# Kernel tuning notes

Measured on AMD Instinct MI355X. Metric: run time of the kernel, lower is better.

Reference implementation:

```python
import jax, jax.numpy as jnp
import numpy as np

B, C, H, W = 8, 192, 128, 128
NH, WS, PS = 6, 8, 8
HD = C // NH
SCALE = HD ** -0.5

def _rel_pos_log(ws):
    # log-spaced signed relative coordinates, [N, N, 2]
    coords = np.stack(np.meshgrid(np.arange(ws), np.arange(ws), indexing='ij'))
    cf = coords.reshape(2, -1)
    rp = (cf[:, :, None] - cf[:, None, :]).transpose(1, 2, 0).astype(np.float32)
    return jnp.asarray(np.sign(rp) * np.log1p(np.abs(rp)))

def setup_inputs() -> dict:
    key = jax.random.key(0)
    ks = jax.random.split(key, 8)
    s = 0.02
    return {
        'x': jax.random.normal(ks[0], (B, C, H, W), jnp.float32),
        'V_w': jax.random.normal(ks[1], (C, C), jnp.float32) * s,
        'V_b': jnp.zeros((C,), jnp.float32),
        'QK_w': jax.random.normal(ks[2], (2 * C, C), jnp.float32) * s,
        'QK_b': jnp.zeros((2 * C,), jnp.float32),
        'proj_w': jax.random.normal(ks[3], (C, C), jnp.float32) * s,
        'proj_b': jnp.zeros((C,), jnp.float32),
        'meta_w1': jax.random.normal(ks[4], (2, 256), jnp.float32) * s,
        'meta_b1': jnp.zeros((256,), jnp.float32),
        'meta_w2': jax.random.normal(ks[5], (256, NH), jnp.float32) * s,
        'meta_b2': jnp.zeros((NH,), jnp.float32),
    }

def reference(x, V_w, V_b, QK_w, QK_b, proj_w, proj_b, meta_w1, meta_b1, meta_w2, meta_b2):
    N = WS * WS
    # 1x1 convs for V and QK
    v = jnp.einsum('bchw,oc->bohw', x, V_w) + V_b[None, :, None, None]
    qk = jnp.einsum('bchw,oc->bohw', x, QK_w) + QK_b[None, :, None, None]
    qkv = jnp.concatenate([qk, v], axis=1)  # [B, 3C, H, W]
    # window partition -> [B * nW, N, 3C]
    t = qkv.transpose(0, 2, 3, 1).reshape(B, H // WS, WS, W // WS, WS, 3 * C)
    wins = t.transpose(0, 1, 3, 2, 4, 5).reshape(-1, N, 3 * C)
    B_ = wins.shape[0]
    qkv3 = wins.reshape(B_, N, 3, NH, HD).transpose(2, 0, 3, 1, 4)
    q, k, vv = qkv3[0] * SCALE, qkv3[1], qkv3[2]  # [B_, NH, N, HD]
    # FFT cross-modulation of q and k over the 8x8 window grid (c = N/64 = 1)
    cg = N // (PS * PS)
    qp = q.reshape(B_, NH, cg, PS, PS, HD).transpose(0, 1, 2, 5, 3, 4)
    kp = k.reshape(B_, NH, cg, PS, PS, HD).transpose(0, 1, 2, 5, 3, 4)
    o = jnp.fft.irfft2(jnp.fft.rfft2(qp) * jnp.fft.rfft2(kp), s=(PS, PS))
    o = o.transpose(0, 1, 2, 4, 5, 3).reshape(B_, NH, N, HD)
    # relative position bias from meta MLP on log-spaced coords
    rp = _rel_pos_log(WS)  # [N, N, 2]
    bias = jax.nn.relu(rp @ meta_w1 + meta_b1) @ meta_w2 + meta_b2  # [N, N, NH]
    bias = bias.transpose(2, 0, 1)  # [NH, N, N]
    attn = jnp.einsum('bhnd,bhmd->bhnm', o, vv) + bias[None]
    attn = jax.nn.softmax(attn, axis=-1)
    y = jnp.einsum('bhnm,bhmd->bhnd', attn, vv).transpose(0, 2, 1, 3).reshape(B_, N, C)
    # window reverse -> [B, C, H, W]
    y = y.reshape(B, H // WS, W // WS, WS, WS, C).transpose(0, 1, 3, 2, 4, 5).reshape(B, H, W, C)
    y = y.transpose(0, 3, 1, 2)
    return jnp.einsum('bchw,oc->bohw', y, proj_w) + proj_b[None, :, None, None]
```

## Files before the change

kernel.cpp:

```cpp
#include <hip/hip_runtime.h>

#define SCALEQ 0.17677669529663687f

typedef __bf16 bf16x8 __attribute__((ext_vector_type(8)));
typedef __bf16 bf16x2 __attribute__((ext_vector_type(2)));
typedef float f32x4 __attribute__((ext_vector_type(4)));
typedef float f32x2 __attribute__((ext_vector_type(2)));

__device__ __forceinline__ float bflo(unsigned int u) { return __uint_as_float(u << 16); }
__device__ __forceinline__ float bfhi(unsigned int u) { return __uint_as_float(u & 0xffff0000u); }
__device__ __forceinline__ f32x2 b2x2(unsigned int u) {
    f32x2 r; r[0] = bflo(u); r[1] = bfhi(u); return r;
}
__device__ __forceinline__ unsigned short f2b(float f) {
    return __builtin_bit_cast(unsigned short, (__bf16)f);
}
__device__ __forceinline__ unsigned int pk2(float a, float b) {
    bf16x2 v; v[0] = (__bf16)a; v[1] = (__bf16)b;
    return __builtin_bit_cast(unsigned int, v);
}

#define RA     0
#define RB     24576
#define RC     49152
#define LDS_BYTES 73728

#define WS_WQKV_ELEMS 110592
#define WS_WP_OFF_EL  110592
#define WS_B2_OFF_B   294912

__device__ __forceinline__ bf16x8 ldsf(const char* p) {
    uint4 u = *(const uint4*)p;
    return __builtin_bit_cast(bf16x8, u);
}
__device__ __forceinline__ bf16x8 gldf(const unsigned short* p) {
    uint4 u = *(const uint4*)p;
    return __builtin_bit_cast(bf16x8, u);
}

__global__ void wprep_kernel(const float* __restrict__ QKw, const float* __restrict__ Vw,
                             const float* __restrict__ Pw, unsigned short* __restrict__ wsb) {
    int i = blockIdx.x * 256 + threadIdx.x;
    if (i >= 147456) return;
    if (i < WS_WQKV_ELEMS) {
        int r = i / 192, c = i - r * 192;
        float v = (r < 384) ? QKw[r * 192 + c] : Vw[(r - 384) * 192 + c];
        if (r < 192) v *= SCALEQ;
        wsb[i] = f2b(v);
    } else {
        int j = i - WS_WQKV_ELEMS;
        wsb[WS_WP_OFF_EL + j] = f2b(Pw[j]);
    }
}

__global__ void bias2_kernel(const float* __restrict__ Mw1, const float* __restrict__ Mb1,
                             const float* __restrict__ Mw2, const float* __restrict__ Mb2,
                             float* __restrict__ out) {
    int i = blockIdx.x * 256 + threadIdx.x;
    if (i >= 6 * 64 * 64) return;
    int h = i >> 12, n = (i >> 6) & 63, m = i & 63;
    float dy = (float)((n >> 3) - (m >> 3));
    float dx = (float)((n & 7) - (m & 7));
    float f0 = copysignf(log1pf(fabsf(dy)), dy);
    float f1 = copysignf(log1pf(fabsf(dx)), dx);
    float a = Mb2[h];
    for (int u = 0; u < 256; ++u) {
        float hv = fmaxf(f0 * Mw1[u] + f1 * Mw1[256 + u] + Mb1[u], 0.0f);
        a = fmaf(hv, Mw2[u * 6 + h], a);
    }
    out[i] = a;
}

__global__ __launch_bounds__(512, 4)
void fused_win_attn(const float* __restrict__ x,
                    const float* __restrict__ Vb, const float* __restrict__ QKb,
                    const float* __restrict__ Pb,
                    const unsigned short* __restrict__ wqkv,
                    const unsigned short* __restrict__ wp,
                    const float* __restrict__ bias2,
                    float* __restrict__ out)
{
    extern __shared__ char smem[];
    const int t   = threadIdx.x;
    const int wv  = t >> 6;
    const int l15 = t & 15;
    const int l4  = (t >> 4) & 3;

    const int wid = ((blockIdx.x & 7) << 8) | (blockIdx.x >> 3);
    const int b   = wid >> 8;
    const int wy  = (wid >> 4) & 15;
    const int wx  = wid & 15;
    const int y0  = wy * 8, x0 = wx * 8;

    const f32x4 zz = {0.0f, 0.0f, 0.0f, 0.0f};

    {
        const float* xb = x + (size_t)b * 192 * 16384;
        #pragma unroll
        for (int i = 0; i < 6; ++i) {
            int idx = t + 512 * i;
            int c = idx >> 4, sub = idx & 15;
            int r = sub >> 1, hf = sub & 1;
            float4 v4 = *(const float4*)(xb + c * 16384 + (y0 + r) * 128 + x0 + hf * 4);
            int n0 = r * 8 + hf * 4;
            unsigned short sv[4] = {f2b(v4.x), f2b(v4.y), f2b(v4.z), f2b(v4.w)};
            #pragma unroll
            for (int e = 0; e < 4; ++e) {
                int n = n0 + e;
                *(unsigned short*)(smem + RA + ((n * 384 + c * 2) ^ ((n & 7) << 4))) = sv[e];
            }
        }
    }
    __syncthreads();

    const int wcol = wv & 3, wrow = wv >> 2;
    unsigned int vp[3][2][2];
    {
        bf16x8 afr[6][2];
        #pragma unroll
        for (int ks = 0; ks < 6; ++ks)
            #pragma unroll
            for (int mtl = 0; mtl < 2; ++mtl) {
                int row = (wrow * 2 + mtl) * 16 + l15;
                afr[ks][mtl] = ldsf(smem + RA + ((row * 384 + ks * 64 + l4 * 16) ^ ((row & 7) << 4)));
            }
        __syncthreads();

        auto gemm3 = [&](int obase, f32x4 acc[3][2]) {
            bf16x8 bw[3][6];
            #pragma unroll
            for (int j = 0; j < 3; ++j) {
                const unsigned short* wr = wqkv + (size_t)(obase + j * 16 + l15) * 192 + l4 * 8;
                #pragma unroll
                for (int ks = 0; ks < 6; ++ks) bw[j][ks] = gldf(wr + ks * 32);
            }
            #pragma unroll
            for (int j = 0; j < 3; ++j) { acc[j][0] = zz; acc[j][1] = zz; }
            #pragma unroll
            for (int ks = 0; ks < 6; ++ks)
                #pragma unroll
                for (int j = 0; j < 3; ++j)
                    #pragma unroll
                    for (int mtl = 0; mtl < 2; ++mtl)
                        acc[j][mtl] = __builtin_amdgcn_mfma_f32_16x16x32_bf16(afr[ks][mtl], bw[j][ks], acc[j][mtl], 0, 0, 0);
        };

        {
            f32x4 acc[3][2];
            gemm3(wcol * 48, acc);
            #pragma unroll
            for (int j = 0; j < 3; ++j) {
                int och = wcol * 48 + j * 16 + l15;
                float bv = QKb[och] * SCALEQ;
                #pragma unroll
                for (int mtl = 0; mtl < 2; ++mtl)
                    #pragma unroll
                    for (int rr = 0; rr < 4; ++rr) {
                        int tok = (wrow * 2 + mtl) * 16 + l4 * 4 + rr;
                        *(unsigned short*)(smem + RA + ((tok * 384 + och * 2) ^ ((tok & 7) << 4)))
                            = f2b(acc[j][mtl][rr] + bv);
                    }
            }
        }
        {
            f32x4 acc[3][2];
            gemm3(192 + wcol * 48, acc);
            #pragma unroll
            for (int j = 0; j < 3; ++j) {
                int ch = wcol * 48 + j * 16 + l15;
                float bv = QKb[192 + ch];
                #pragma unroll
                for (int mtl = 0; mtl < 2; ++mtl)
                    #pragma unroll
                    for (int rr = 0; rr < 4; ++rr) {
                        int tok = (wrow * 2 + mtl) * 16 + l4 * 4 + rr;
                        *(unsigned short*)(smem + RB + ((tok * 384 + ch * 2) ^ ((tok & 7) << 4)))
                            = f2b(acc[j][mtl][rr] + bv);
                    }
            }
        }
        {
            f32x4 acc[3][2];
            gemm3(384 + wcol * 48, acc);
            #pragma unroll
            for (int j = 0; j < 3; ++j) {
                int ch = wcol * 48 + j * 16 + l15;
                float bv = Vb[ch];
                #pragma unroll
                for (int mtl = 0; mtl < 2; ++mtl) {
                    vp[j][mtl][0] = pk2(acc[j][mtl][0] + bv, acc[j][mtl][1] + bv);
                    vp[j][mtl][1] = pk2(acc[j][mtl][2] + bv, acc[j][mtl][3] + bv);
                }
            }
        }
    }
    __syncthreads();

    if (t < 384) {
        const int rn = t / 48, cc = t % 48;
        const int c0b = cc * 8;
        f32x2 acc[8][2];
        #pragma unroll
        for (int cn = 0; cn < 8; ++cn) {
            acc[cn][0] = (f32x2){0.0f, 0.0f};
            acc[cn][1] = (f32x2){0.0f, 0.0f};
        }
        #pragma unroll
        for (int kh = 0; kh < 2; ++kh) {
            uint2 karr[32];
            #pragma unroll
            for (int m = 0; m < 32; ++m) {
                int row = kh * 32 + m;
                karr[m] = *(const uint2*)(smem + RB + ((row * 384 + c0b) ^ ((row & 7) << 4)));
            }
            #pragma unroll
            for (int mrl = 0; mrl < 4; ++mrl) {
                const int mr = kh * 4 + mrl;
                f32x2 kf[8][2];
                #pragma unroll
                for (int mc = 0; mc < 8; ++mc) {
                    uint2 kv = karr[mrl * 8 + mc];
                    kf[mc][0] = b2x2(kv.x); kf[mc][1] = b2x2(kv.y);
                }
                const int npr = (rn - mr) & 7;
                #pragma unroll
                for (int npc = 0; npc < 8; ++npc) {
                    int np = npr * 8 + npc;
                    uint2 qv = *(const uint2*)(smem + RA + ((np * 384 + c0b) ^ ((np & 7) << 4)));
                    f32x2 qf0 = b2x2(qv.x), qf1 = b2x2(qv.y);
                    #pragma unroll
                    for (int mc = 0; mc < 8; ++mc) {
                        int cn = (npc + mc) & 7;
                        acc[cn][0] = qf0 * kf[mc][0] + acc[cn][0];
                        acc[cn][1] = qf1 * kf[mc][1] + acc[cn][1];
                    }
                }
            }
        }
        #pragma unroll
        for (int cn = 0; cn < 8; ++cn) {
            int n = rn * 8 + cn;
            uint2 pk;
            pk.x = pk2(acc[cn][0][0], acc[cn][0][1]);
            pk.y = pk2(acc[cn][1][0], acc[cn][1][1]);
            *(uint2*)(smem + RC + ((n * 384 + c0b) ^ ((n & 7) << 4))) = pk;
        }
    }
    __syncthreads();

    {
        #pragma unroll
        for (int j = 0; j < 3; ++j) {
            int ch = wcol * 48 + j * 16 + l15;
            #pragma unroll
            for (int mtl = 0; mtl < 2; ++mtl)
                #pragma unroll
                for (int pp = 0; pp < 2; ++pp) {
                    unsigned int pk = vp[j][mtl][pp];
                    int tok0 = (wrow * 2 + mtl) * 16 + l4 * 4 + pp * 2;
                    *(unsigned int*)(smem + RB + ((ch * 128 + tok0 * 2) ^ ((ch & 7) << 4))) = pk;
                    *(unsigned short*)(smem + RA + ((tok0 * 384 + ch * 2) ^ ((tok0 & 7) << 4)))
                        = (unsigned short)(pk & 0xffffu);
                    *(unsigned short*)(smem + RA + (((tok0 + 1) * 384 + ch * 2) ^ (((tok0 + 1) & 7) << 4)))
                        = (unsigned short)(pk >> 16);
                }
        }
    }
    __syncthreads();

    unsigned int pv[3][4][2];
    {
        #pragma unroll
        for (int i = 0; i < 3; ++i) {
            int u = wv * 3 + i;
            int h = u >> 2, nt = u & 3;
            int brow = nt * 16 + l15;
            bf16x8 ofr = ldsf(smem + RC + ((brow * 384 + h * 64 + l4 * 16) ^ ((brow & 7) << 4)));
            int n = nt * 16 + l15;
            const float* bp = bias2 + ((h * 64 + n) << 6) + l4 * 4;
            float s[4][4];
            #pragma unroll
            for (int mt = 0; mt < 4; ++mt) {
                int arow = mt * 16 + l15;
                bf16x8 vfr = ldsf(smem + RA + ((arow * 384 + h * 64 + l4 * 16) ^ ((arow & 7) << 4)));
                f32x4 a = __builtin_amdgcn_mfma_f32_16x16x32_bf16(vfr, ofr, zz, 0, 0, 0);
                float4 bb = *(const float4*)(bp + mt * 16);
                s[mt][0] = a[0] + bb.x; s[mt][1] = a[1] + bb.y;
                s[mt][2] = a[2] + bb.z; s[mt][3] = a[3] + bb.w;
            }
            float m0 = s[0][0];
            #pragma unroll
            for (int mt = 0; mt < 4; ++mt)
                #pragma unroll
                for (int rr = 0; rr < 4; ++rr) m0 = fmaxf(m0, s[mt][rr]);
            m0 = fmaxf(m0, __shfl_xor(m0, 16));
            m0 = fmaxf(m0, __shfl_xor(m0, 32));
            float sm = 0.0f;
            #pragma unroll
            for (int mt = 0; mt < 4; ++mt)
                #pragma unroll
                for (int rr = 0; rr < 4; ++rr) {
                    float p = __expf(s[mt][rr] - m0);
                    s[mt][rr] = p; sm += p;
                }
            sm += __shfl_xor(sm, 16);
            sm += __shfl_xor(sm, 32);
            float inv = 1.0f / sm;
            #pragma unroll
            for (int mt = 0; mt < 4; ++mt) {
                pv[i][mt][0] = pk2(s[mt][0] * inv, s[mt][1] * inv);
                pv[i][mt][1] = pk2(s[mt][2] * inv, s[mt][3] * inv);
            }
        }
    }
    __syncthreads();

    {
        #pragma unroll
        for (int i = 0; i < 3; ++i) {
            int u = wv * 3 + i;
            int h = u >> 2, nt = u & 3;
            bf16x8 pafr[2];
            #pragma unroll
            for (int ks = 0; ks < 2; ++ks) {
                unsigned int au[4];
                #pragma unroll
                for (int p = 0; p < 4; ++p) {
                    int srcl4 = (2 * l4 + (p >> 1)) & 3;
                    int src = srcl4 * 16 + l15;
                    unsigned int v0 = (unsigned int)__shfl((int)pv[i][2 * ks][p & 1], src, 64);
                    unsigned int v1 = (unsigned int)__shfl((int)pv[i][2 * ks + 1][p & 1], src, 64);
                    au[p] = (l4 & 2) ? v1 : v0;
                }
                uint4 u4 = {au[0], au[1], au[2], au[3]};
                pafr[ks] = __builtin_bit_cast(bf16x8, u4);
            }
            f32x4 acc[2];
            acc[0] = zz; acc[1] = zz;
            #pragma unroll
            for (int dt = 0; dt < 2; ++dt)
                #pragma unroll
                for (int ks = 0; ks < 2; ++ks) {
                    int drow = h * 32 + dt * 16 + l15;
                    bf16x8 vtf = ldsf(smem + RB + ((drow * 128 + ks * 64 + l4 * 16) ^ ((drow & 7) << 4)));
                    acc[dt] = __builtin_amdgcn_mfma_f32_16x16x32_bf16(pafr[ks], vtf, acc[dt], 0, 0, 0);
                }
            #pragma unroll
            for (int dt = 0; dt < 2; ++dt)
                #pragma unroll
                for (int rr = 0; rr < 4; ++rr) {
                    int tok = nt * 16 + l4 * 4 + rr;
                    int ch  = h * 32 + dt * 16 + l15;
                    *(unsigned short*)(smem + RC + ((tok * 384 + ch * 2) ^ ((tok & 7) << 4))) = f2b(acc[dt][rr]);
                }
        }
    }
    __syncthreads();

    {
        const int wc = wv & 3, wr = wv >> 2;
        bf16x8 wfr[3][6];
        #pragma unroll
        for (int jt = 0; jt < 3; ++jt) {
            int oc = wc * 48 + jt * 16;
            const unsigned short* wr_ = wp + (size_t)(oc + l15) * 192 + l4 * 8;
            #pragma unroll
            for (int ks = 0; ks < 6; ++ks) wfr[jt][ks] = gldf(wr_ + ks * 32);
        }
        f32x4 acc[3][2];
        #pragma unroll
        for (int jt = 0; jt < 3; ++jt) { acc[jt][0] = zz; acc[jt][1] = zz; }

        #pragma unroll
        for (int ks = 0; ks < 6; ++ks) {
            bf16x8 bfr[2];
            #pragma unroll
            for (int ntl = 0; ntl < 2; ++ntl) {
                int tok = (wr * 2 + ntl) * 16 + l15;
                bfr[ntl] = ldsf(smem + RC + ((tok * 384 + ks * 64 + l4 * 16) ^ ((tok & 7) << 4)));
            }
            #pragma unroll
            for (int jt = 0; jt < 3; ++jt)
                #pragma unroll
                for (int ntl = 0; ntl < 2; ++ntl)
                    acc[jt][ntl] = __builtin_amdgcn_mfma_f32_16x16x32_bf16(wfr[jt][ks], bfr[ntl], acc[jt][ntl], 0, 0, 0);
        }
        #pragma unroll
        for (int jt = 0; jt < 3; ++jt)
            #pragma unroll
            for (int rr = 0; rr < 4; ++rr) {
                int oc = wc * 48 + jt * 16 + l4 * 4 + rr;
                float pb = Pb[oc];
                float* obase = out + (size_t)(b * 192 + oc) * 16384;
                #pragma unroll
                for (int ntl = 0; ntl < 2; ++ntl) {
                    int tok = (wr * 2 + ntl) * 16 + l15;
                    __builtin_nontemporal_store(acc[jt][ntl][rr] + pb,
                        obase + (y0 + (tok >> 3)) * 128 + x0 + (tok & 7));
                }
            }
    }
}

extern "C" void kernel_launch(void* const* d_in, const int* in_sizes, int n_in,
                              void* d_out, int out_size, void* d_ws, size_t ws_size,
                              hipStream_t stream) {
    const float* x   = (const float*)d_in[0];
    const float* Vw  = (const float*)d_in[1];
    const float* Vb  = (const float*)d_in[2];
    const float* QKw = (const float*)d_in[3];
    const float* QKb = (const float*)d_in[4];
    const float* Pw  = (const float*)d_in[5];
    const float* Pb  = (const float*)d_in[6];
    const float* Mw1 = (const float*)d_in[7];
    const float* Mb1 = (const float*)d_in[8];
    const float* Mw2 = (const float*)d_in[9];
    const float* Mb2 = (const float*)d_in[10];
    float* outp = (float*)d_out;

    unsigned short* wsb = (unsigned short*)d_ws;
    float* b2 = (float*)((char*)d_ws + WS_B2_OFF_B);

    wprep_kernel<<<dim3(576), dim3(256), 0, stream>>>(QKw, Vw, Pw, wsb);
    bias2_kernel<<<dim3(96), dim3(256), 0, stream>>>(Mw1, Mb1, Mw2, Mb2, b2);

    (void)hipFuncSetAttribute((const void*)fused_win_attn,
                              hipFuncAttributeMaxDynamicSharedMemorySize, LDS_BYTES);
    fused_win_attn<<<dim3(2048), dim3(512), LDS_BYTES, stream>>>(
        x, Vb, QKb, Pb, wsb, wsb + WS_WP_OFF_EL, b2, outp);
}
```

Before: 307.2 us.

## Split output projection into a separate row-wise kernel via bf16 workspace

When the workspace is large enough, the fused attention kernel writes per-window attention output as bf16 to a global buffer and exits. A new proj_kernel then processes one full image row per block, so the final NCHW stores are contiguous 128-float rows instead of scattered 8-element window segments. This trades an extra round trip through global memory for the intermediate (about 50 MB) and an extra launch against better-coalesced output writes. The fallback fused path also switches from nontemporal to regular stores.

```diff
diff --git a/kernel.cpp b/kernel.cpp
--- a/kernel.cpp
+++ b/kernel.cpp
@@ -28,6 +28,8 @@
 #define WS_WQKV_ELEMS 110592
 #define WS_WP_OFF_EL  110592
 #define WS_B2_OFF_B   294912
+#define WS_YB_OFF_B   393216
+#define WS_TOTAL_B    50724864
 
 __device__ __forceinline__ bf16x8 ldsf(const char* p) {
     uint4 u = *(const uint4*)p;
@@ -78,7 +80,9 @@
                     const unsigned short* __restrict__ wqkv,
                     const unsigned short* __restrict__ wp,
                     const float* __restrict__ bias2,
-                    float* __restrict__ out)
+                    unsigned short* __restrict__ yb,
+                    float* __restrict__ out,
+                    int split)
 {
     extern __shared__ char smem[];
     const int t   = threadIdx.x;
@@ -345,16 +349,29 @@
                     bf16x8 vtf = ldsf(smem + RB + ((drow * 128 + ks * 64 + l4 * 16) ^ ((drow & 7) << 4)));
                     acc[dt] = __builtin_amdgcn_mfma_f32_16x16x32_bf16(pafr[ks], vtf, acc[dt], 0, 0, 0);
                 }
-            #pragma unroll
-            for (int dt = 0; dt < 2; ++dt)
-                #pragma unroll
-                for (int rr = 0; rr < 4; ++rr) {
-                    int tok = nt * 16 + l4 * 4 + rr;
-                    int ch  = h * 32 + dt * 16 + l15;
-                    *(unsigned short*)(smem + RC + ((tok * 384 + ch * 2) ^ ((tok & 7) << 4))) = f2b(acc[dt][rr]);
-                }
-        }
-    }
+            if (split) {
+                unsigned short* ybw = yb + (size_t)wid * 64 * 192;
+                #pragma unroll
+                for (int dt = 0; dt < 2; ++dt)
+                    #pragma unroll
+                    for (int rr = 0; rr < 4; ++rr) {
+                        int tok = nt * 16 + l4 * 4 + rr;
+                        int ch  = h * 32 + dt * 16 + l15;
+                        ybw[tok * 192 + ch] = f2b(acc[dt][rr]);
+                    }
+            } else {
+                #pragma unroll
+                for (int dt = 0; dt < 2; ++dt)
+                    #pragma unroll
+                    for (int rr = 0; rr < 4; ++rr) {
+                        int tok = nt * 16 + l4 * 4 + rr;
+                        int ch  = h * 32 + dt * 16 + l15;
+                        *(unsigned short*)(smem + RC + ((tok * 384 + ch * 2) ^ ((tok & 7) << 4))) = f2b(acc[dt][rr]);
+                    }
+            }
+        }
+    }
+    if (split) return;
     __syncthreads();
 
     {
@@ -395,8 +412,83 @@
                 #pragma unroll
                 for (int ntl = 0; ntl < 2; ++ntl) {
                     int tok = (wr * 2 + ntl) * 16 + l15;
-                    __builtin_nontemporal_store(acc[jt][ntl][rr] + pb,
-                        obase + (y0 + (tok >> 3)) * 128 + x0 + (tok & 7));
+                    obase[(y0 + (tok >> 3)) * 128 + x0 + (tok & 7)] = acc[jt][ntl][rr] + pb;
+                }
+            }
+    }
+}
+
+__global__ __launch_bounds__(256)
+void proj_kernel(const unsigned short* __restrict__ yb,
+                 const unsigned short* __restrict__ wp,
+                 const float* __restrict__ Pb,
+                 float* __restrict__ out)
+{
+    extern __shared__ char smem[];
+    const int t   = threadIdx.x;
+    const int wv  = t >> 6;
+    const int l15 = t & 15;
+    const int l4  = (t >> 4) & 3;
+
+    const int by = blockIdx.x;
+    const int b  = by >> 7;
+    const int y  = by & 127;
+    const int wy = y >> 3, row = y & 7;
+
+    const f32x4 zz = {0.0f, 0.0f, 0.0f, 0.0f};
+
+    #pragma unroll
+    for (int k = 0; k < 12; ++k) {
+        int i = t + 256 * k;
+        int px = i / 24, cb = i % 24;
+        int wx = px >> 3, col = px & 7;
+        const unsigned short* src = yb
+            + ((size_t)(((b * 16 + wy) * 16 + wx) * 64 + row * 8 + col)) * 192 + cb * 8;
+        uint4 v = *(const uint4*)src;
+        *(uint4*)(smem + ((px * 384 + cb * 16) ^ ((px & 7) << 4))) = v;
+    }
+    __syncthreads();
+
+    bf16x8 wfr[3][6];
+    #pragma unroll
+    for (int jt = 0; jt < 3; ++jt) {
+        int oc = wv * 48 + jt * 16;
+        const unsigned short* wr_ = wp + (size_t)(oc + l15) * 192 + l4 * 8;
+        #pragma unroll
+        for (int ks = 0; ks < 6; ++ks) wfr[jt][ks] = gldf(wr_ + ks * 32);
+    }
+    #pragma unroll
+    for (int half = 0; half < 2; ++half) {
+        f32x4 acc[3][4];
+        #pragma unroll
+        for (int jt = 0; jt < 3; ++jt)
+            #pragma unroll
+            for (int ntl = 0; ntl < 4; ++ntl) acc[jt][ntl] = zz;
+        #pragma unroll
+        for (int ks = 0; ks < 6; ++ks) {
+            bf16x8 bfr[4];
+            #pragma unroll
+            for (int ntl = 0; ntl < 4; ++ntl) {
+                int px = (half * 4 + ntl) * 16 + l15;
+                bfr[ntl] = ldsf(smem + ((px * 384 + ks * 64 + l4 * 16) ^ ((px & 7) << 4)));
+            }
+            #pragma unroll
+            for (int jt = 0; jt < 3; ++jt)
+                #pragma unroll
+                for (int ntl = 0; ntl < 4; ++ntl)
+                    acc[jt][ntl] = __builtin_amdgcn_mfma_f32_16x16x32_bf16(wfr[jt][ks], bfr[ntl], acc[jt][ntl], 0, 0, 0);
+        }
+        #pragma unroll
+        for (int jt = 0; jt < 3; ++jt)
+            #pragma unroll
+            for (int rr = 0; rr < 4; ++rr) {
+                int oc = wv * 48 + jt * 16 + l4 * 4 + rr;
+                float pb = Pb[oc];
+                float* op = out + ((size_t)(b * 192 + oc) * 128 + y) * 128;
+                #pragma unroll
+                for (int ntl = 0; ntl < 4; ++ntl) {
+                    int px = (half * 4 + ntl) * 16 + l15;
+                    op[px] = acc[jt][ntl][rr] + pb;
                 }
             }
     }
@@ -420,6 +512,8 @@
 
     unsigned short* wsb = (unsigned short*)d_ws;
     float* b2 = (float*)((char*)d_ws + WS_B2_OFF_B);
+    unsigned short* ybp = (unsigned short*)((char*)d_ws + WS_YB_OFF_B);
+    const int split = (ws_size >= (size_t)WS_TOTAL_B) ? 1 : 0;
 
     wprep_kernel<<<dim3(576), dim3(256), 0, stream>>>(QKw, Vw, Pw, wsb);
     bias2_kernel<<<dim3(96), dim3(256), 0, stream>>>(Mw1, Mb1, Mw2, Mb2, b2);
@@ -427,5 +521,12 @@
     (void)hipFuncSetAttribute((const void*)fused_win_attn,
                               hipFuncAttributeMaxDynamicSharedMemorySize, LDS_BYTES);
     fused_win_attn<<<dim3(2048), dim3(512), LDS_BYTES, stream>>>(
-        x, Vb, QKb, Pb, wsb, wsb + WS_WP_OFF_EL, b2, outp);
-}
+        x, Vb, QKb, Pb, wsb, wsb + WS_WP_OFF_EL, b2, ybp, outp, split);
+
+    if (split) {
+        (void)hipFuncSetAttribute((const void*)proj_kernel,
+                                  hipFuncAttributeMaxDynamicSharedMemorySize, 49152);
+        proj_kernel<<<dim3(1024), dim3(256), 49152, stream>>>(
+            ybp, wsb + WS_WP_OFF_EL, Pb, outp);
+    }
+}
```

Result: faster. 292.8 us (-4.7%).
